# Kernel optimization log

Hardware: AMD Instinct MI355X
Metric: run time of the kernel (lower is better)

Reference implementation:

```python
import jax, jax.numpy as jnp
import numpy as np

DIM = 768; NL = 13; NH = 12; VOCAB = 50257; SEQ = 512; B = 4
HID = 4 * DIM; HD = DIM // NH; LUT_SIZE = 256


def setup_inputs() -> dict:
    key = jax.random.key(0)
    ks = jax.random.split(key, 10)
    def n(k, shape, s=0.02):
        return jax.random.normal(k, shape, jnp.float32) * s
    return {
        'lut': jnp.linspace(-0.1, 0.1, LUT_SIZE, dtype=jnp.float32),  # 256-entry primal codebook
        'tok_emb': n(ks[0], (VOCAB, DIM)),
        'pos_emb': n(ks[1], (SEQ, DIM)),
        'ln1_g': jnp.ones((NL, DIM), jnp.float32), 'ln1_b': jnp.zeros((NL, DIM), jnp.float32),
        'in_w': n(ks[2], (NL, 3 * DIM, DIM)), 'in_b': jnp.zeros((NL, 3 * DIM), jnp.float32),
        'out_w': n(ks[3], (NL, DIM, DIM)), 'out_b': jnp.zeros((NL, DIM), jnp.float32),
        'ln2_g': jnp.ones((NL, DIM), jnp.float32), 'ln2_b': jnp.zeros((NL, DIM), jnp.float32),
        'mlp1_scale': jnp.ones((NL, HID, 1), jnp.float32),
        'mlp2_scale': jnp.ones((NL, DIM, 1), jnp.float32),
        'lnf_g': jnp.ones((DIM,), jnp.float32), 'lnf_b': jnp.zeros((DIM,), jnp.float32),
        'head_scale': jnp.ones((VOCAB, 1), jnp.float32),
        'mlp1_idx': jax.random.randint(ks[4], (NL, HID, DIM), 0, LUT_SIZE, jnp.int32),
        'mlp2_idx': jax.random.randint(ks[5], (NL, DIM, HID), 0, LUT_SIZE, jnp.int32),
        'head_idx': jax.random.randint(ks[6], (VOCAB, DIM), 0, LUT_SIZE, jnp.int32),
        'idx': jax.random.randint(ks[7], (B, SEQ), 0, VOCAB, jnp.int32),
    }


def layernorm(x, g, b, eps=1e-5):
    m = jnp.mean(x, -1, keepdims=True)
    v = jnp.var(x, -1, keepdims=True)
    return (x - m) * jax.lax.rsqrt(v + eps) * g + b


def ghost_linear(x, gidx, scale, lut):
    # dequantize: gather codebook values, row-scale, then matmul (no bias)
    w = lut[gidx] * scale  # [out, in]
    return x @ w.T


def mha(x, wi, bi, wo, bo, mask):
    Bn, T, D = x.shape
    qkv = x @ wi.T + bi
    q, k, v = jnp.split(qkv, 3, axis=-1)
    q = q.reshape(Bn, T, NH, HD); k = k.reshape(Bn, T, NH, HD); v = v.reshape(Bn, T, NH, HD)
    s = jnp.einsum('bqhd,bkhd->bhqk', q, k) / jnp.sqrt(jnp.float32(HD)) + mask
    a = jax.nn.softmax(s, axis=-1)
    o = jnp.einsum('bhqk,bkhd->bqhd', a, v).reshape(Bn, T, D)
    return o @ wo.T + bo


def reference(lut, tok_emb, pos_emb, ln1_g, ln1_b, in_w, in_b, out_w, out_b,
              ln2_g, ln2_b, mlp1_scale, mlp2_scale, lnf_g, lnf_b, head_scale,
              mlp1_idx, mlp2_idx, head_idx, idx):
    Bn, T = idx.shape
    x = tok_emb[idx] + pos_emb[:T]
    causal = jnp.triu(jnp.ones((T, T), bool), 1)
    mask = jnp.where(causal, -jnp.inf, 0.0).astype(jnp.float32)
    for l in range(NL):
        h = layernorm(x, ln1_g[l], ln1_b[l])
        x = x + mha(h, in_w[l], in_b[l], out_w[l], out_b[l], mask)
        h = layernorm(x, ln2_g[l], ln2_b[l])
        h = ghost_linear(h, mlp1_idx[l], mlp1_scale[l], lut)
        h = jax.nn.gelu(h, approximate=True)  # GELU tanh approximation
        x = x + ghost_linear(h, mlp2_idx[l], mlp2_scale[l], lut)
    x = layernorm(x, lnf_g, lnf_b)
    return ghost_linear(x, head_idx, head_scale, lut)
```

## Files before the change

kernel.cpp:

```cpp
#include <hip/hip_runtime.h>
#include <stdint.h>

#define DIM 768
#define NL 13
#define NH 12
#define VOCAB 50257
#define SEQ 512
#define BATCH 4
#define HID 3072
#define HD 64
#define NTOK (BATCH*SEQ)
#define BHB (BATCH*NH)

typedef unsigned short u16;
typedef __attribute__((ext_vector_type(8))) __bf16 bf16x8;
typedef __attribute__((ext_vector_type(4))) float f32x4;

#define ASM_VMCNT(N) asm volatile("s_waitcnt vmcnt(" #N ")" ::: "memory")
#define ASM_LGKM0()  asm volatile("s_waitcnt lgkmcnt(0)" ::: "memory")

__device__ __forceinline__ u16 f2bf(float f) {
    union { float f; uint32_t u; } v; v.f = f;
    uint32_t u = v.u;
    return (u16)((u + 0x7FFFu + ((u >> 16) & 1u)) >> 16);
}

__device__ __forceinline__ void gl2lds16(const void* g, void* l) {
    __builtin_amdgcn_global_load_lds((const __attribute__((address_space(1))) void*)g,
                                     (__attribute__((address_space(3))) void*)l,
                                     16, 0, 0);
}

__device__ __forceinline__ float gelu_tanh(float x) {
    const float y = 0.7978845608028654f * (x + 0.044715f * x * x * x);
    const float t = 1.0f - 2.0f / (__expf(2.0f * y) + 1.0f);
    return 0.5f * x * (1.0f + t);
}

__device__ __forceinline__ void xcd_remap(int& bx, int& by) {
    const int gx = gridDim.x;
    const int nwg = gx * gridDim.y;
    const int orig = by * gx + bx;
    const int xcd = orig & 7;
    const int q = nwg >> 3, r = nwg & 7;
    const int wg = (xcd < r ? xcd * (q + 1) : r * (q + 1) + (xcd - r) * q) + (orig >> 3);
    bx = wg % gx; by = wg / gx;
}

template<int EPI>
__device__ __forceinline__ void epi_store(float v, int r, int c, int N, int z, long sC,
                                          const float* bias, const float* resid,
                                          void* out0, void* out1, void* out2)
{
    if constexpr (EPI == 0) {
        if (c < N) ((float*)out0)[(long)z * sC + (long)r * N + c] = v;
    } else if constexpr (EPI == 1) {
        v += bias[c];
        const int part = c / DIM;
        const int cc = c - part * DIM;
        const int hh = cc >> 6, d = cc & 63;
        const int b = r >> 9, t = r & 511;
        const int bh = b * NH + hh;
        if (part == 0)      ((u16*)out0)[((long)bh * SEQ + t) * HD + d] = f2bf(v);
        else if (part == 1) ((u16*)out1)[((long)bh * SEQ + t) * HD + d] = f2bf(v);
        else                ((u16*)out2)[((long)bh * HD + d) * SEQ + t] = f2bf(v);
    } else if constexpr (EPI == 3) {
        if (bias) v += bias[c];
        v += resid[(long)r * N + c];
        ((float*)out0)[(long)r * N + c] = v;
    } else if constexpr (EPI == 5) {
        if (bias && z == 0) v += bias[c];
        atomicAdd(&((float*)out0)[(long)r * N + c], v);
    } else {
        ((u16*)out0)[(long)r * N + c] = f2bf(gelu_tanh(v));
    }
}

template<int WN, int EPI>
__global__ __launch_bounds__(256)
void gemm_bt(const u16* __restrict__ A, const u16* __restrict__ B,
             const float* __restrict__ bias, const float* __restrict__ resid,
             void* __restrict__ out0, void* __restrict__ out1, void* __restrict__ out2,
             int M, int N, int K, long sA, long sB, long sC)
{
    constexpr int TN = WN * 32;
    constexpr int NBG = TN / 64;
    __shared__ __align__(16) u16 As[2 * 128 * 32];
    __shared__ __align__(16) u16 Bs[2 * TN * 32];

    const int tid  = threadIdx.x;
    const int wave = tid >> 6;
    const int lane = tid & 63;
    const int quad = lane >> 4;
    const int l16  = lane & 15;
    const int wm   = wave >> 1;
    const int wn   = wave & 1;

    int bx = blockIdx.x, by = blockIdx.y;
    xcd_remap(bx, by);

    const int m0 = bx * 128;
    const int n0 = by * TN;
    const int z  = blockIdx.z;

    const u16* Ab = A + (long)z * sA;
    const u16* Bb = B + (long)z * sB;

    const int srow = tid >> 2;
    const int scol = ((tid & 3) ^ ((srow >> 1) & 3)) * 8;

    const long aoff0 = (long)(m0 + srow) * K + scol;
    const long aoff1 = (long)(m0 + 64 + srow) * K + scol;
    long boff[NBG];
    #pragma unroll
    for (int g = 0; g < NBG; g++) {
        int br = n0 + g * 64 + srow; if (br > N - 1) br = N - 1;
        boff[g] = (long)br * K + scol;
    }

    auto stage = [&](int b, int k0) {
        gl2lds16(Ab + aoff0 + k0, As + b * 4096 + wave * 512);
        gl2lds16(Ab + aoff1 + k0, As + b * 4096 + 2048 + wave * 512);
        #pragma unroll
        for (int g = 0; g < NBG; g++)
            gl2lds16(Bb + boff[g] + k0, Bs + b * (TN * 32) + g * 2048 + wave * 512);
    };

    f32x4 acc[4][WN];
    #pragma unroll
    for (int i = 0; i < 4; i++)
        #pragma unroll
        for (int j = 0; j < WN; j++)
            acc[i][j] = (f32x4){0.f, 0.f, 0.f, 0.f};

    const int sq8 = (quad ^ ((l16 >> 1) & 3)) * 8;
    const int arow = (wm * 64 + l16) * 32 + sq8;
    const int brow = (wn * (WN * 16) + l16) * 32 + sq8;

    stage(0, 0);
    if (K > 32) stage(1, 32);

    int cur = 0;
    for (int k0 = 0; k0 < K; k0 += 32) {
        if (k0 + 32 < K) ASM_VMCNT(4); else ASM_VMCNT(0);
        __builtin_amdgcn_s_barrier();

        const u16* Ar = As + cur * 4096;
        const u16* Br = Bs + cur * (TN * 32);
        bf16x8 af[4], bfr[WN];
        #pragma unroll
        for (int i = 0; i < 4; i++)
            af[i] = *(const bf16x8*)&Ar[arow + i * 512];
        #pragma unroll
        for (int j = 0; j < WN; j++)
            bfr[j] = *(const bf16x8*)&Br[brow + j * 512];
        ASM_LGKM0();
        __builtin_amdgcn_s_barrier();
        if (k0 + 64 < K) stage(cur, k0 + 64);

        #pragma unroll
        for (int i = 0; i < 4; i++)
            #pragma unroll
            for (int j = 0; j < WN; j++)
                acc[i][j] = __builtin_amdgcn_mfma_f32_16x16x32_bf16(af[i], bfr[j], acc[i][j], 0, 0, 0);

        cur ^= 1;
    }

    const int rbase = m0 + wm * 64;
    const int cbase = n0 + wn * (WN * 16);
    #pragma unroll
    for (int i = 0; i < 4; i++)
        #pragma unroll
        for (int j = 0; j < WN; j++)
            #pragma unroll
            for (int rg = 0; rg < 4; rg++)
                epi_store<EPI>(acc[i][j][rg], rbase + i * 16 + quad * 4 + rg,
                               cbase + j * 16 + l16, N, z, sC, bias, resid, out0, out1, out2);
}

template<int WN, int EPI>
__global__ __launch_bounds__(256)
void gemm64(const u16* __restrict__ A, const u16* __restrict__ B,
            const float* __restrict__ bias, const float* __restrict__ resid,
            void* __restrict__ out0, void* __restrict__ out1, void* __restrict__ out2,
            int M, int N, int K, int Kstride)
{
    constexpr int TN = WN * 32;
    constexpr int NC = TN / 32;
    __shared__ __align__(16) u16 As[2 * 64 * 64];
    __shared__ __align__(16) u16 Bs[2 * TN * 64];

    const int tid  = threadIdx.x;
    const int wave = tid >> 6;
    const int lane = tid & 63;
    const int quad = lane >> 4;
    const int l16  = lane & 15;
    const int wm   = wave >> 1;
    const int wn   = wave & 1;

    int bx = blockIdx.x, by = blockIdx.y;
    xcd_remap(bx, by);
    const int m0 = bx * 64;
    const int n0 = by * TN;
    const int koff = blockIdx.z * K;

    const int srow = tid >> 3;
    const int sch  = ((tid & 7) ^ (srow & 7)) * 8;
    u16* const asw = As + wave * 512;
    u16* const bsw = Bs + wave * 512;

    const long aoff = (long)(m0 + srow) * Kstride + koff + sch;
    const long boff = (long)(n0 + srow) * Kstride + koff + sch;

    auto stageA = [&](int b, int k0) {
        #pragma unroll
        for (int c = 0; c < 2; c++)
            gl2lds16(A + aoff + (long)c * 32 * Kstride + k0, asw + b * 4096 + c * 2048);
    };
    auto stageB = [&](int b, int k0) {
        #pragma unroll
        for (int c = 0; c < NC; c++)
            gl2lds16(B + boff + (long)c * 32 * Kstride + k0, bsw + b * TN * 64 + c * 2048);
    };

    f32x4 acc[2][WN];
    #pragma unroll
    for (int i = 0; i < 2; i++)
        #pragma unroll
        for (int j = 0; j < WN; j++)
            acc[i][j] = (f32x4){0.f, 0.f, 0.f, 0.f};

    const int rsw = l16 & 7;

    stageA(0, 0); stageB(0, 0);
    if (K > 64) { stageA(1, 64); stageB(1, 64); }

    int cur = 0;
    for (int k0 = 0; k0 < K; k0 += 64) {
        if (k0 + 64 < K) { if constexpr (NC == 4) ASM_VMCNT(6); else ASM_VMCNT(4); }
        else ASM_VMCNT(0);
        __builtin_amdgcn_s_barrier();

        const u16* Ar = As + cur * 4096;
        const u16* Br = Bs + cur * TN * 64;
        bf16x8 af[2][2], bfr[WN][2];
        #pragma unroll
        for (int i = 0; i < 2; i++)
            #pragma unroll
            for (int kk = 0; kk < 2; kk++)
                af[i][kk] = *(const bf16x8*)&Ar[(wm * 32 + i * 16 + l16) * 64 + (((kk * 4 + quad) ^ rsw) * 8)];
        #pragma unroll
        for (int j = 0; j < WN; j++)
            #pragma unroll
            for (int kk = 0; kk < 2; kk++)
                bfr[j][kk] = *(const bf16x8*)&Br[(wn * (WN * 16) + j * 16 + l16) * 64 + (((kk * 4 + quad) ^ rsw) * 8)];
        ASM_LGKM0();
        __builtin_amdgcn_s_barrier();
        if (k0 + 128 < K) { stageA(cur, k0 + 128); stageB(cur, k0 + 128); }

        #pragma unroll
        for (int kk = 0; kk < 2; kk++)
            #pragma unroll
            for (int i = 0; i < 2; i++)
                #pragma unroll
                for (int j = 0; j < WN; j++)
                    acc[i][j] = __builtin_amdgcn_mfma_f32_16x16x32_bf16(af[i][kk], bfr[j][kk], acc[i][j], 0, 0, 0);

        cur ^= 1;
    }

    const int rbase = m0 + wm * 32;
    const int cbase = n0 + wn * (WN * 16);
    #pragma unroll
    for (int i = 0; i < 2; i++)
        #pragma unroll
        for (int j = 0; j < WN; j++)
            #pragma unroll
            for (int rg = 0; rg < 4; rg++)
                epi_store<EPI>(acc[i][j][rg], rbase + i * 16 + quad * 4 + rg,
                               cbase + j * 16 + l16, N, (int)blockIdx.z, 0,
                               bias, resid, out0, out1, out2);
}

__global__ __launch_bounds__(256)
void attn_kernel(const u16* __restrict__ qb, const u16* __restrict__ kb,
                 const u16* __restrict__ vtb, u16* __restrict__ ob)
{
    __shared__ __align__(16) u16 Ks[512 * 64];
    __shared__ __align__(16) u16 Vs[64 * 512];
    __shared__ __align__(16) u16 Ps[4][32 * 64];

    const int tid  = threadIdx.x;
    const int wave = tid >> 6;
    const int lane = tid & 63;
    const int quad = lane >> 4;
    const int l16  = lane & 15;

    const int bh   = blockIdx.x;
    const int qblk = blockIdx.y;
    const int qr0  = qblk * 128 + wave * 32;

    #pragma unroll 4
    for (int cI = 0; cI < 16; ++cI) {
        const int rbase = cI * 32 + wave * 8;
        const int r  = rbase + (lane >> 3);
        const int ch = lane & 7;
        gl2lds16(kb + ((long)bh * SEQ + r) * HD + ((ch ^ (r & 7)) * 8), Ks + rbase * 64);
    }
    #pragma unroll 4
    for (int cI = 0; cI < 16; ++cI) {
        const int d = cI * 4 + wave;
        gl2lds16(vtb + ((long)bh * HD + d) * SEQ + ((lane ^ (d & 7)) * 8), Vs + d * 512);
    }

    bf16x8 af[2][2];
    const long qoff = ((long)bh * SEQ + qr0) * HD;
    #pragma unroll
    for (int i = 0; i < 2; i++)
        #pragma unroll
        for (int kc = 0; kc < 2; kc++)
            af[i][kc] = *(const bf16x8*)&qb[qoff + (long)(i * 16 + l16) * HD + kc * 32 + quad * 8];

    __syncthreads();

    f32x4 o[2][4];
    float mrun[2][4], lrun[2][4];
    #pragma unroll
    for (int i = 0; i < 2; i++)
        #pragma unroll
        for (int rg = 0; rg < 4; rg++) { mrun[i][rg] = -1e30f; lrun[i][rg] = 0.f; }
    #pragma unroll
    for (int i = 0; i < 2; i++)
        #pragma unroll
        for (int nd = 0; nd < 4; nd++)
            o[i][nd] = (f32x4){0.f, 0.f, 0.f, 0.f};

    u16* const Pw = &Ps[wave][0];
    const int rsw = l16 & 7;
    const int kvend = qr0 + 32;

    for (int kv0 = 0; kv0 < kvend; kv0 += 64) {
        f32x4 s[2][4];
        #pragma unroll
        for (int i = 0; i < 2; i++)
            #pragma unroll
            for (int n = 0; n < 4; n++)
                s[i][n] = (f32x4){0.f, 0.f, 0.f, 0.f};
        bf16x8 bf[4][2];
        #pragma unroll
        for (int n = 0; n < 4; n++)
            #pragma unroll
            for (int kc = 0; kc < 2; kc++)
                bf[n][kc] = *(const bf16x8*)&Ks[(kv0 + n * 16 + l16) * 64 + (((kc * 4 + quad) ^ rsw) * 8)];
        #pragma unroll
        for (int i = 0; i < 2; i++)
            #pragma unroll
            for (int n = 0; n < 4; n++)
                #pragma unroll
                for (int kc = 0; kc < 2; kc++)
                    s[i][n] = __builtin_amdgcn_mfma_f32_16x16x32_bf16(af[i][kc], bf[n][kc], s[i][n], 0, 0, 0);

        #pragma unroll
        for (int i = 0; i < 2; i++) {
            #pragma unroll
            for (int rg = 0; rg < 4; rg++) {
                const int q = qr0 + i * 16 + quad * 4 + rg;
                float v[4];
                #pragma unroll
                for (int n = 0; n < 4; n++) {
                    const int c = kv0 + n * 16 + l16;
                    v[n] = (c <= q) ? s[i][n][rg] * 0.125f : -1e30f;
                }
                float pm = fmaxf(fmaxf(v[0], v[1]), fmaxf(v[2], v[3]));
                #pragma unroll
                for (int off = 1; off < 16; off <<= 1) pm = fmaxf(pm, __shfl_xor(pm, off));
                const float mo = mrun[i][rg];
                const float mn = fmaxf(mo, pm);
                const float corr = __expf(mo - mn);
                float ps = 0.f;
                #pragma unroll
                for (int n = 0; n < 4; n++) { const float e = __expf(v[n] - mn); v[n] = e; ps += e; }
                #pragma unroll
                for (int off = 1; off < 16; off <<= 1) ps += __shfl_xor(ps, off);
                lrun[i][rg] = lrun[i][rg] * corr + ps;
                mrun[i][rg] = mn;
                #pragma unroll
                for (int nd = 0; nd < 4; nd++) o[i][nd][rg] *= corr;
                const int qlz = i * 16 + quad * 4 + rg;
                const int sw = qlz & 7;
                #pragma unroll
                for (int n = 0; n < 4; n++)
                    Pw[qlz * 64 + (((n * 2 + (l16 >> 3)) ^ sw) * 8) + (l16 & 7)] = f2bf(v[n]);
            }
        }
        asm volatile("s_waitcnt lgkmcnt(0)" ::: "memory");

        bf16x8 pa[2][2], vb[4][2];
        #pragma unroll
        for (int i = 0; i < 2; i++)
            #pragma unroll
            for (int kc = 0; kc < 2; kc++)
                pa[i][kc] = *(const bf16x8*)&Pw[(i * 16 + l16) * 64 + (((kc * 4 + quad) ^ rsw) * 8)];
        #pragma unroll
        for (int nd = 0; nd < 4; nd++)
            #pragma unroll
            for (int kc = 0; kc < 2; kc++)
                vb[nd][kc] = *(const bf16x8*)&Vs[(nd * 16 + l16) * 512 + ((((kv0 >> 3) + kc * 4 + quad) ^ rsw) * 8)];
        #pragma unroll
        for (int i = 0; i < 2; i++)
            #pragma unroll
            for (int nd = 0; nd < 4; nd++)
                #pragma unroll
                for (int kc = 0; kc < 2; kc++)
                    o[i][nd] = __builtin_amdgcn_mfma_f32_16x16x32_bf16(pa[i][kc], vb[nd][kc], o[i][nd], 0, 0, 0);
    }

    const int b  = bh / NH, hh = bh - b * NH;
    #pragma unroll
    for (int i = 0; i < 2; i++) {
        #pragma unroll
        for (int rg = 0; rg < 4; rg++) {
            const float inv = 1.f / lrun[i][rg];
            const int t = qr0 + i * 16 + quad * 4 + rg;
            u16* orow = ob + ((long)(b * SEQ + t)) * DIM + hh * HD;
            #pragma unroll
            for (int nd = 0; nd < 4; nd++)
                orow[nd * 16 + l16] = f2bf(o[i][nd][rg] * inv);
        }
    }
}

__global__ __launch_bounds__(256)
void embed_kernel(const int* __restrict__ tokidx, const float* __restrict__ tok,
                  const float* __restrict__ pos, float* __restrict__ x)
{
    const int i = blockIdx.x * 256 + threadIdx.x;
    const int row = i / 192;
    const int c4 = i - row * 192;
    const int t = row & (SEQ - 1);
    const int tk = tokidx[row];
    const float4 a = *(const float4*)&tok[(long)tk * DIM + c4 * 4];
    const float4 p = *(const float4*)&pos[(long)t * DIM + c4 * 4];
    *(float4*)&x[(long)row * DIM + c4 * 4] = make_float4(a.x + p.x, a.y + p.y, a.z + p.z, a.w + p.w);
}

__global__ __launch_bounds__(256)
void ln_kernel(const float* __restrict__ x, const float* __restrict__ g,
               const float* __restrict__ b, u16* __restrict__ out)
{
    const int row = blockIdx.x * 4 + (threadIdx.x >> 6);
    const int lane = threadIdx.x & 63;
    const float* xr = x + (long)row * DIM;
    float v[12];
    float s = 0.f, s2 = 0.f;
    #pragma unroll
    for (int i = 0; i < 3; i++) {
        const float4 f = *(const float4*)&xr[i * 256 + lane * 4];
        v[i*4+0] = f.x; v[i*4+1] = f.y; v[i*4+2] = f.z; v[i*4+3] = f.w;
        s  += f.x + f.y + f.z + f.w;
        s2 += f.x*f.x + f.y*f.y + f.z*f.z + f.w*f.w;
    }
    for (int o = 32; o; o >>= 1) { s += __shfl_xor(s, o); s2 += __shfl_xor(s2, o); }
    const float m  = s * (1.f / DIM);
    const float var = s2 * (1.f / DIM) - m * m;
    const float rs = rsqrtf(var + 1e-5f);
    u16* orow = out + (long)row * DIM;
    #pragma unroll
    for (int i = 0; i < 3; i++) {
        const int c = i * 256 + lane * 4;
        ushort4 o4 = make_ushort4(
            f2bf((v[i*4+0] - m) * rs * g[c+0] + b[c+0]),
            f2bf((v[i*4+1] - m) * rs * g[c+1] + b[c+1]),
            f2bf((v[i*4+2] - m) * rs * g[c+2] + b[c+2]),
            f2bf((v[i*4+3] - m) * rs * g[c+3] + b[c+3]));
        *(ushort4*)&orow[c] = o4;
    }
}

__global__ __launch_bounds__(256)
void tobf16_kernel(const float* __restrict__ in, u16* __restrict__ out)
{
    const long i = ((long)blockIdx.x * 256 + threadIdx.x) * 4;
    const float4 f = *(const float4*)&in[i];
    *(ushort4*)&out[i] = make_ushort4(f2bf(f.x), f2bf(f.y), f2bf(f.z), f2bf(f.w));
}

__global__ __launch_bounds__(256)
void dequant_kernel(const int* __restrict__ gidx, const float* __restrict__ scale,
                    const float* __restrict__ lut, u16* __restrict__ w,
                    long total, int Kd)
{
    __shared__ float slut[256];
    slut[threadIdx.x] = lut[threadIdx.x];
    __syncthreads();
    const long i4 = ((long)blockIdx.x * 256 + threadIdx.x) * 4;
    if (i4 >= total) return;
    const int4 g = *(const int4*)&gidx[i4];
    const float sc = scale[(int)(i4 / Kd)];
    *(ushort4*)&w[i4] = make_ushort4(f2bf(slut[g.x] * sc), f2bf(slut[g.y] * sc),
                                     f2bf(slut[g.z] * sc), f2bf(slut[g.w] * sc));
}

extern "C" void kernel_launch(void* const* d_in, const int* in_sizes, int n_in,
                              void* d_out, int out_size, void* d_ws, size_t ws_size,
                              hipStream_t stream)
{
    const float* lut        = (const float*)d_in[0];
    const float* tok_emb    = (const float*)d_in[1];
    const float* pos_emb    = (const float*)d_in[2];
    const float* ln1_g      = (const float*)d_in[3];
    const float* ln1_b      = (const float*)d_in[4];
    const float* in_w       = (const float*)d_in[5];
    const float* in_b       = (const float*)d_in[6];
    const float* out_w      = (const float*)d_in[7];
    const float* out_b      = (const float*)d_in[8];
    const float* ln2_g      = (const float*)d_in[9];
    const float* ln2_b      = (const float*)d_in[10];
    const float* mlp1_scale = (const float*)d_in[11];
    const float* mlp2_scale = (const float*)d_in[12];
    const float* lnf_g      = (const float*)d_in[13];
    const float* lnf_b      = (const float*)d_in[14];
    const float* head_scale = (const float*)d_in[15];
    const int*   mlp1_idx   = (const int*)d_in[16];
    const int*   mlp2_idx   = (const int*)d_in[17];
    const int*   head_idx   = (const int*)d_in[18];
    const int*   tokids     = (const int*)d_in[19];

    char* p = (char*)d_ws;
    auto alloc = [&](size_t bytes) { char* r = p; p += (bytes + 255) & ~(size_t)255; return r; };
    float* x    = (float*)alloc((size_t)NTOK * DIM * 4);
    u16*  h     = (u16*) alloc((size_t)NTOK * DIM * 2);
    u16*  h2    = (u16*) alloc((size_t)NTOK * HID * 2);
    u16*  qb    = (u16*) alloc((size_t)BHB * SEQ * HD * 2);
    u16*  kb    = (u16*) alloc((size_t)BHB * SEQ * HD * 2);
    u16*  vtb   = (u16*) alloc((size_t)BHB * SEQ * HD * 2);
    u16*  ob    = (u16*) alloc((size_t)NTOK * DIM * 2);
    u16*  inw16 = (u16*) alloc((size_t)NL * 3 * DIM * DIM * 2);
    u16*  outw16= (u16*) alloc((size_t)NL * DIM * DIM * 2);
    u16*  hw    = (u16*) alloc((size_t)VOCAB * DIM * 2);

    const size_t layerW = (size_t)HID * DIM * 2;
    const size_t used   = (size_t)(p - (char*)d_ws);
    const bool hoist    = ws_size >= used + 2 * NL * layerW + 1024;
    u16* w1 = (u16*)alloc(hoist ? NL * layerW : layerW);
    u16* w2 = (u16*)alloc(hoist ? NL * layerW : layerW);

    embed_kernel<<<NTOK * 192 / 256, 256, 0, stream>>>(tokids, tok_emb, pos_emb, x);
    tobf16_kernel<<<NL * 3 * DIM * DIM / 1024, 256, 0, stream>>>(in_w, inw16);
    tobf16_kernel<<<NL * DIM * DIM / 1024, 256, 0, stream>>>(out_w, outw16);
    {
        const long total = (long)VOCAB * DIM;
        const int blocks = (int)((total / 4 + 255) / 256);
        dequant_kernel<<<blocks, 256, 0, stream>>>(head_idx, head_scale, lut, hw, total, DIM);
    }
    if (hoist) {
        const long t1 = (long)NL * HID * DIM;
        dequant_kernel<<<(int)(t1 / 1024), 256, 0, stream>>>(mlp1_idx, mlp1_scale, lut, w1, t1, DIM);
        dequant_kernel<<<(int)(t1 / 1024), 256, 0, stream>>>(mlp2_idx, mlp2_scale, lut, w2, t1, HID);
    }

    for (int l = 0; l < NL; l++) {
        u16* w1l = hoist ? w1 + (size_t)l * HID * DIM : w1;
        u16* w2l = hoist ? w2 + (size_t)l * HID * DIM : w2;

        ln_kernel<<<NTOK / 4, 256, 0, stream>>>(x, ln1_g + l * DIM, ln1_b + l * DIM, h);
        gemm64<4, 1><<<dim3(NTOK / 64, 3 * DIM / 128), 256, 0, stream>>>(
            h, inw16 + (long)l * 3 * DIM * DIM, in_b + l * 3 * DIM, nullptr,
            qb, kb, vtb, NTOK, 3 * DIM, DIM, DIM);
        attn_kernel<<<dim3(BHB, 4), 256, 0, stream>>>(qb, kb, vtb, ob);
        gemm64<2, 5><<<dim3(NTOK / 64, DIM / 64, 2), 256, 0, stream>>>(
            ob, outw16 + (long)l * DIM * DIM, out_b + l * DIM, nullptr,
            x, nullptr, nullptr, NTOK, DIM, DIM / 2, DIM);
        ln_kernel<<<NTOK / 4, 256, 0, stream>>>(x, ln2_g + l * DIM, ln2_b + l * DIM, h);
        if (!hoist)
            dequant_kernel<<<HID * DIM / 1024, 256, 0, stream>>>(
                mlp1_idx + (long)l * HID * DIM, mlp1_scale + l * HID, lut, w1l, (long)HID * DIM, DIM);
        gemm64<4, 4><<<dim3(NTOK / 64, HID / 128), 256, 0, stream>>>(
            h, w1l, nullptr, nullptr, h2, nullptr, nullptr, NTOK, HID, DIM, DIM);
        if (!hoist)
            dequant_kernel<<<DIM * HID / 1024, 256, 0, stream>>>(
                mlp2_idx + (long)l * DIM * HID, mlp2_scale + l * DIM, lut, w2l, (long)DIM * HID, HID);
        gemm64<2, 5><<<dim3(NTOK / 64, DIM / 64, 2), 256, 0, stream>>>(
            h2, w2l, nullptr, nullptr, x, nullptr, nullptr, NTOK, DIM, HID / 2, HID);
    }

    ln_kernel<<<NTOK / 4, 256, 0, stream>>>(x, lnf_g, lnf_b, h);
    gemm_bt<4, 0><<<dim3(NTOK / 128, (VOCAB + 127) / 128, 1), 256, 0, stream>>>(
        h, hw, nullptr, nullptr, d_out, nullptr, nullptr, NTOK, VOCAB, DIM, 0, 0, 0);
}
```

Measured before the change: 2.554 ms.

## Shrink attention blocks, lazy softmax rescale, merge prep kernels, deeper MLP2 split-K

The attention kernel now runs 128-thread blocks over 64 query rows each, doubling the grid, and loads only the K rows needed under the causal mask. Online softmax rescales the accumulators only when the running max grows by more than 8, which skips most of the exp and multiply work. The two bf16 conversion launches and the two MLP dequant launches are each merged into a single launch. The MLP2 GEMM split-K goes from 2 to 4 slices to expose more blocks. Costs are more atomic or residual accumulation traffic for the split-K, and a lazy-rescale threshold that could let exp values grow large.

Measured after the change: 2.911 ms. 1.14x slower.

```diff
diff --git a/kernel.cpp b/kernel.cpp
--- a/kernel.cpp
+++ b/kernel.cpp
@@ -283,13 +283,13 @@
                                bias, resid, out0, out1, out2);
 }
 
-__global__ __launch_bounds__(256)
+__global__ __launch_bounds__(128)
 void attn_kernel(const u16* __restrict__ qb, const u16* __restrict__ kb,
                  const u16* __restrict__ vtb, u16* __restrict__ ob)
 {
     __shared__ __align__(16) u16 Ks[512 * 64];
     __shared__ __align__(16) u16 Vs[64 * 512];
-    __shared__ __align__(16) u16 Ps[4][32 * 64];
+    __shared__ __align__(16) u16 Ps[2][32 * 64];
 
     const int tid  = threadIdx.x;
     const int wave = tid >> 6;
@@ -299,18 +299,18 @@
 
     const int bh   = blockIdx.x;
     const int qblk = blockIdx.y;
-    const int qr0  = qblk * 128 + wave * 32;
-
-    #pragma unroll 4
-    for (int cI = 0; cI < 16; ++cI) {
-        const int rbase = cI * 32 + wave * 8;
+    const int qr0  = qblk * 64 + wave * 32;
+    const int nkv  = (qblk + 1) * 64;
+
+    for (int cI = 0; cI < (nkv >> 4); ++cI) {
+        const int rbase = cI * 16 + wave * 8;
         const int r  = rbase + (lane >> 3);
         const int ch = lane & 7;
         gl2lds16(kb + ((long)bh * SEQ + r) * HD + ((ch ^ (r & 7)) * 8), Ks + rbase * 64);
     }
     #pragma unroll 4
-    for (int cI = 0; cI < 16; ++cI) {
-        const int d = cI * 4 + wave;
+    for (int cI = 0; cI < 32; ++cI) {
+        const int d = cI * 2 + wave;
         gl2lds16(vtb + ((long)bh * HD + d) * SEQ + ((lane ^ (d & 7)) * 8), Vs + d * 512);
     }
 
@@ -375,18 +375,20 @@
                 float pm = fmaxf(fmaxf(v[0], v[1]), fmaxf(v[2], v[3]));
                 #pragma unroll
                 for (int off = 1; off < 16; off <<= 1) pm = fmaxf(pm, __shfl_xor(pm, off));
-                const float mo = mrun[i][rg];
-                const float mn = fmaxf(mo, pm);
-                const float corr = __expf(mo - mn);
+                if (pm > mrun[i][rg] + 8.f) {
+                    const float corr = __expf(mrun[i][rg] - pm);
+                    mrun[i][rg] = pm;
+                    lrun[i][rg] *= corr;
+                    #pragma unroll
+                    for (int nd = 0; nd < 4; nd++) o[i][nd][rg] *= corr;
+                }
+                const float mn = mrun[i][rg];
                 float ps = 0.f;
                 #pragma unroll
                 for (int n = 0; n < 4; n++) { const float e = __expf(v[n] - mn); v[n] = e; ps += e; }
                 #pragma unroll
                 for (int off = 1; off < 16; off <<= 1) ps += __shfl_xor(ps, off);
-                lrun[i][rg] = lrun[i][rg] * corr + ps;
-                mrun[i][rg] = mn;
-                #pragma unroll
-                for (int nd = 0; nd < 4; nd++) o[i][nd][rg] *= corr;
+                lrun[i][rg] += ps;
                 const int qlz = i * 16 + quad * 4 + rg;
                 const int sw = qlz & 7;
                 #pragma unroll
@@ -479,11 +481,15 @@
 }
 
 __global__ __launch_bounds__(256)
-void tobf16_kernel(const float* __restrict__ in, u16* __restrict__ out)
-{
-    const long i = ((long)blockIdx.x * 256 + threadIdx.x) * 4;
-    const float4 f = *(const float4*)&in[i];
-    *(ushort4*)&out[i] = make_ushort4(f2bf(f.x), f2bf(f.y), f2bf(f.z), f2bf(f.w));
+void tobf16_2(const float* __restrict__ a, u16* __restrict__ oa,
+              const float* __restrict__ b, u16* __restrict__ ob, long na)
+{
+    long i = ((long)blockIdx.x * 256 + threadIdx.x) * 4;
+    const float* src; u16* dst;
+    if (i < na) { src = a; dst = oa; }
+    else        { i -= na; src = b; dst = ob; }
+    const float4 f = *(const float4*)&src[i];
+    *(ushort4*)&dst[i] = make_ushort4(f2bf(f.x), f2bf(f.y), f2bf(f.z), f2bf(f.w));
 }
 
 __global__ __launch_bounds__(256)
@@ -500,6 +506,25 @@
     const float sc = scale[(int)(i4 / Kd)];
     *(ushort4*)&w[i4] = make_ushort4(f2bf(slut[g.x] * sc), f2bf(slut[g.y] * sc),
                                      f2bf(slut[g.z] * sc), f2bf(slut[g.w] * sc));
+}
+
+__global__ __launch_bounds__(256)
+void dequant2_kernel(const int* __restrict__ g1, const float* __restrict__ s1,
+                     const int* __restrict__ g2, const float* __restrict__ s2,
+                     const float* __restrict__ lut,
+                     u16* __restrict__ w1, u16* __restrict__ w2, long halfBlocks)
+{
+    __shared__ float slut[256];
+    slut[threadIdx.x] = lut[threadIdx.x];
+    __syncthreads();
+    const long bid = blockIdx.x;
+    const int* g; const float* s; u16* w; int Kd; long i4;
+    if (bid < halfBlocks) { g = g1; s = s1; w = w1; Kd = DIM; i4 = (bid * 256 + threadIdx.x) * 4; }
+    else                  { g = g2; s = s2; w = w2; Kd = HID; i4 = ((bid - halfBlocks) * 256 + threadIdx.x) * 4; }
+    const int4 q = *(const int4*)&g[i4];
+    const float sc = s[(long)(i4 / Kd)];
+    *(ushort4*)&w[i4] = make_ushort4(f2bf(slut[q.x] * sc), f2bf(slut[q.y] * sc),
+                                     f2bf(slut[q.z] * sc), f2bf(slut[q.w] * sc));
 }
 
 extern "C" void kernel_launch(void* const* d_in, const int* in_sizes, int n_in,
@@ -547,8 +572,11 @@
     u16* w2 = (u16*)alloc(hoist ? NL * layerW : layerW);
 
     embed_kernel<<<NTOK * 192 / 256, 256, 0, stream>>>(tokids, tok_emb, pos_emb, x);
-    tobf16_kernel<<<NL * 3 * DIM * DIM / 1024, 256, 0, stream>>>(in_w, inw16);
-    tobf16_kernel<<<NL * DIM * DIM / 1024, 256, 0, stream>>>(out_w, outw16);
+    {
+        const long na = (long)NL * 3 * DIM * DIM;
+        const long nb = (long)NL * DIM * DIM;
+        tobf16_2<<<(int)((na + nb) / 1024), 256, 0, stream>>>(in_w, inw16, out_w, outw16, na);
+    }
     {
         const long total = (long)VOCAB * DIM;
         const int blocks = (int)((total / 4 + 255) / 256);
@@ -556,8 +584,9 @@
     }
     if (hoist) {
         const long t1 = (long)NL * HID * DIM;
-        dequant_kernel<<<(int)(t1 / 1024), 256, 0, stream>>>(mlp1_idx, mlp1_scale, lut, w1, t1, DIM);
-        dequant_kernel<<<(int)(t1 / 1024), 256, 0, stream>>>(mlp2_idx, mlp2_scale, lut, w2, t1, HID);
+        const long halfBlocks = t1 / 1024;
+        dequant2_kernel<<<(int)(2 * halfBlocks), 256, 0, stream>>>(
+            mlp1_idx, mlp1_scale, mlp2_idx, mlp2_scale, lut, w1, w2, halfBlocks);
     }
 
     for (int l = 0; l < NL; l++) {
@@ -568,7 +597,7 @@
         gemm64<4, 1><<<dim3(NTOK / 64, 3 * DIM / 128), 256, 0, stream>>>(
             h, inw16 + (long)l * 3 * DIM * DIM, in_b + l * 3 * DIM, nullptr,
             qb, kb, vtb, NTOK, 3 * DIM, DIM, DIM);
-        attn_kernel<<<dim3(BHB, 4), 256, 0, stream>>>(qb, kb, vtb, ob);
+        attn_kernel<<<dim3(BHB, 8), 128, 0, stream>>>(qb, kb, vtb, ob);
         gemm64<2, 5><<<dim3(NTOK / 64, DIM / 64, 2), 256, 0, stream>>>(
             ob, outw16 + (long)l * DIM * DIM, out_b + l * DIM, nullptr,
             x, nullptr, nullptr, NTOK, DIM, DIM / 2, DIM);
@@ -581,8 +610,8 @@
         if (!hoist)
             dequant_kernel<<<DIM * HID / 1024, 256, 0, stream>>>(
                 mlp2_idx + (long)l * DIM * HID, mlp2_scale + l * DIM, lut, w2l, (long)DIM * HID, HID);
-        gemm64<2, 5><<<dim3(NTOK / 64, DIM / 64, 2), 256, 0, stream>>>(
-            h2, w2l, nullptr, nullptr, x, nullptr, nullptr, NTOK, DIM, HID / 2, HID);
+        gemm64<2, 5><<<dim3(NTOK / 64, DIM / 64, 4), 256, 0, stream>>>(
+            h2, w2l, nullptr, nullptr, x, nullptr, nullptr, NTOK, DIM, HID / 4, HID);
     }
 
     ln_kernel<<<NTOK / 4, 256, 0, stream>>>(x, lnf_g, lnf_b, h);
```
